# Performance work log

Measured on AMD Instinct MI355X. Metric: run time of the kernel, lower is better.

The kernel has to match this reference:

```python
import jax, jax.numpy as jnp
import numpy as np

H = 4096
T = 8192
EPS = 1e-06
BLK = 16  # NVFP4 block size (per-16-element fp8 block scales)

# representable magnitudes of FP4 e2m1 and midpoints for round-to-nearest
FP4_VALS = jnp.array([0.0, 0.5, 1.0, 1.5, 2.0, 3.0, 4.0, 6.0], dtype=jnp.float32)
FP4_MIDS = jnp.array([0.25, 0.75, 1.25, 1.75, 2.5, 3.5, 5.0], dtype=jnp.float32)
FP8_MAX = 448.0  # e4m3fn max


def fp4_round(x):
    """Round to nearest FP4 (e2m1) value, saturating at +/-6."""
    s = jnp.sign(x)
    a = jnp.clip(jnp.abs(x), 0.0, 6.0)
    idx = jnp.searchsorted(FP4_MIDS, a, side='right')
    return s * FP4_VALS[idx]


def fp4_quant(x, gs):
    """Emulates vllm scaled_fp4_quant: per-16-elem fp8(e4m3) block scales with a
    global fp32 scale gs. Returns (q_blocks [M, K/16, 16], scale [M, K/16, 1]).
    Dequant relation: x ~= q * scale / gs."""
    M, K = x.shape
    xb = x.reshape(M, K // BLK, BLK)
    amax = jnp.max(jnp.abs(xb), axis=-1, keepdims=True)
    sc = jnp.clip(amax / 6.0 * gs, 0.0, FP8_MAX)
    sc = sc.astype(jnp.float8_e4m3fn).astype(jnp.float32)  # fp8 rounding of block scale
    safe_sc = jnp.where(sc > 0, sc, 1.0)
    q = fp4_round(jnp.where(sc > 0, xb * gs / safe_sc, 0.0))
    return q, sc


def fp4_mm(aq, asc, bq, bsc, alpha):
    """Emulates cutlass_scaled_fp4_mm: out = (Aq*asc) @ (Bq*bsc)^T * alpha,
    where alpha = 1/(a_global_scale * b_global_scale)."""
    M = aq.shape[0]
    N = bq.shape[0]
    A = (aq * asc).reshape(M, -1)
    B = (bq * bsc).reshape(N, -1)
    return (A @ B.T) * alpha


def rmsnorm(x, w, eps=EPS):
    return x * jax.lax.rsqrt(jnp.mean(x * x, axis=-1, keepdims=True) + eps) * w


def setup_inputs() -> dict:
    key = jax.random.key(0)
    ks = jax.random.split(key, 5)
    hidden_states = jax.random.normal(ks[0], (T, H), dtype=jnp.float32)
    norm_w = jax.random.uniform(ks[1], (4, H), dtype=jnp.float32)
    w = jax.random.uniform(ks[2], (3, H, H), dtype=jnp.float32)
    agscale = jax.random.uniform(ks[3], (3,), dtype=jnp.float32)
    wgscale = jax.random.uniform(ks[4], (3,), dtype=jnp.float32)
    return dict(hidden_states=hidden_states, norm_w=norm_w, w=w,
                agscale=agscale, wgscale=wgscale)


def reference(hidden_states, norm_w, w, agscale, wgscale):
    # tensor_model_parallel_all_reduce is identity on a single device
    x = jax.nn.relu(hidden_states)
    resid = x
    y = rmsnorm(x, norm_w[0])
    for i in range(3):
        wq, wsc = fp4_quant(w[i], wgscale[i])      # weight quant (done at init in torch)
        yq, ysc = fp4_quant(y, agscale[i])          # activation static quant
        alpha = 1.0 / (wgscale[i] * agscale[i])
        z = fp4_mm(yq, ysc, wq, wsc, alpha)         # [T, H]
        x = z + resid                                # fused add RMSNorm
        resid = x
        y = rmsnorm(x, norm_w[i + 1])
    return y
```

## Files before the change

### kernel.cpp

```cpp
#include <hip/hip_runtime.h>

constexpr int HD = 4096;
constexpr int TD = 8192;

typedef __bf16 bf16;
typedef __bf16 bf16x4 __attribute__((ext_vector_type(4)));
typedef __bf16 bf16x8 __attribute__((ext_vector_type(8)));
typedef float  f32x4  __attribute__((ext_vector_type(4)));

__device__ __forceinline__ float e4m3_round(float v) {
    if (!(v > 0.0f)) return 0.0f;
    unsigned b = __float_as_uint(v);
    int exp = (int)((b >> 23) & 255) - 127;
    int shift = (exp < -6) ? -9 : (exp - 3);
    float sc  = __uint_as_float((unsigned)(127 + shift) << 23);
    float isc = __uint_as_float((unsigned)(127 - shift) << 23);
    return rintf(v * isc) * sc;
}

__device__ __forceinline__ float fp4_round(float x) {
    float s = (x < 0.0f) ? -1.0f : 1.0f;
    float a = fminf(fabsf(x), 6.0f);
    float v;
    if      (a < 0.25f) v = 0.0f;
    else if (a < 0.75f) v = 0.5f;
    else if (a < 1.25f) v = 1.0f;
    else if (a < 1.75f) v = 1.5f;
    else if (a < 2.5f)  v = 2.0f;
    else if (a < 3.5f)  v = 3.0f;
    else if (a < 5.0f)  v = 4.0f;
    else                v = 6.0f;
    return s * v;
}

__device__ __forceinline__ void load_lds16(const void* g, void* l) {
    typedef __attribute__((address_space(1))) const void gv_t;
    typedef __attribute__((address_space(3))) void lv_t;
    __builtin_amdgcn_global_load_lds((gv_t*)g, (lv_t*)l, 16, 0, 0);
}

__global__ __launch_bounds__(256) void quant_w_kernel(
        const float* __restrict__ w, const float* __restrict__ wg,
        bf16* __restrict__ bdeq) {
    const size_t t4 = (size_t)blockIdx.x * 256 + threadIdx.x;
    const int mat = (int)(t4 >> 22);
    const float gs = wg[mat];
    const float4 v = ((const float4*)w)[t4];
    float am = fmaxf(fmaxf(fabsf(v.x), fabsf(v.y)), fmaxf(fabsf(v.z), fabsf(v.w)));
    am = fmaxf(am, __shfl_xor(am, 1));
    am = fmaxf(am, __shfl_xor(am, 2));
    const float sc = e4m3_round(fminf((am / 6.0f) * gs, 448.0f));
    bf16x4 o;
    if (sc > 0.0f) {
        o[0] = (bf16)(fp4_round(v.x * gs / sc) * sc);
        o[1] = (bf16)(fp4_round(v.y * gs / sc) * sc);
        o[2] = (bf16)(fp4_round(v.z * gs / sc) * sc);
        o[3] = (bf16)(fp4_round(v.w * gs / sc) * sc);
    } else {
        o[0] = o[1] = o[2] = o[3] = (bf16)0.0f;
    }
    ((bf16x4*)bdeq)[t4] = o;
}

__global__ __launch_bounds__(256) void rms_quant_kernel(
        const float* __restrict__ in, float* __restrict__ resid_out,
        const float* __restrict__ nw, const float* __restrict__ gsp,
        bf16* __restrict__ qout, float* __restrict__ yout, const int mode) {
    const int row  = blockIdx.x;
    const int tid  = threadIdx.x;
    const int lane = tid & 63;
    const int wave = tid >> 6;
    const float* x = in + (size_t)row * HD;

    float4 v[4];
    float ss = 0.0f;
#pragma unroll
    for (int c = 0; c < 4; c++) {
        v[c] = ((const float4*)x)[c * 256 + tid];
        if (mode == 0) {
            v[c].x = fmaxf(v[c].x, 0.0f);
            v[c].y = fmaxf(v[c].y, 0.0f);
            v[c].z = fmaxf(v[c].z, 0.0f);
            v[c].w = fmaxf(v[c].w, 0.0f);
        }
        ss += v[c].x * v[c].x + v[c].y * v[c].y + v[c].z * v[c].z + v[c].w * v[c].w;
    }
    if (mode == 0) {
        float4* r = (float4*)(resid_out + (size_t)row * HD);
#pragma unroll
        for (int c = 0; c < 4; c++) r[c * 256 + tid] = v[c];
    }
#pragma unroll
    for (int m = 1; m < 64; m <<= 1) ss += __shfl_xor(ss, m);
    __shared__ float sred[4];
    if (lane == 0) sred[wave] = ss;
    __syncthreads();
    const float total = sred[0] + sred[1] + sred[2] + sred[3];
    const float rs = rsqrtf(total * (1.0f / HD) + 1e-6f);
    const float gs = (mode == 2) ? 0.0f : *gsp;

#pragma unroll
    for (int c = 0; c < 4; c++) {
        const float4 nv = ((const float4*)nw)[c * 256 + tid];
        float4 y;
        y.x = v[c].x * rs * nv.x;
        y.y = v[c].y * rs * nv.y;
        y.z = v[c].z * rs * nv.z;
        y.w = v[c].w * rs * nv.w;
        if (mode == 2) {
            ((float4*)(yout + (size_t)row * HD))[c * 256 + tid] = y;
        } else {
            float am = fmaxf(fmaxf(fabsf(y.x), fabsf(y.y)), fmaxf(fabsf(y.z), fabsf(y.w)));
            am = fmaxf(am, __shfl_xor(am, 1));
            am = fmaxf(am, __shfl_xor(am, 2));
            const float sc = e4m3_round(fminf((am / 6.0f) * gs, 448.0f));
            bf16x4 o;
            if (sc > 0.0f) {
                o[0] = (bf16)(fp4_round(y.x * gs / sc) * sc);
                o[1] = (bf16)(fp4_round(y.y * gs / sc) * sc);
                o[2] = (bf16)(fp4_round(y.z * gs / sc) * sc);
                o[3] = (bf16)(fp4_round(y.w * gs / sc) * sc);
            } else {
                o[0] = o[1] = o[2] = o[3] = (bf16)0.0f;
            }
            ((bf16x4*)(qout + (size_t)row * HD))[c * 256 + tid] = o;
        }
    }
}

__global__ __launch_bounds__(256) void gemm_bt_kernel(
        const bf16* __restrict__ A, const bf16* __restrict__ B,
        float* __restrict__ C,
        const float* __restrict__ agp, const float* __restrict__ wgp) {
    __shared__ __align__(16) bf16 sA[128 * 32];
    __shared__ __align__(16) bf16 sB[128 * 32];

    const int tid  = threadIdx.x;
    const int lane = tid & 63;
    const int wave = tid >> 6;
    const int tileM = blockIdx.x * 128;
    const int tileN = blockIdx.y * 128;
    const int waveM = (wave & 1) * 64;
    const int waveN = (wave >> 1) * 64;
    const int quad = lane >> 4;
    const int l16  = lane & 15;

    const float alpha = 1.0f / ((*wgp) * (*agp));

    f32x4 acc[4][4];
#pragma unroll
    for (int mi = 0; mi < 4; mi++)
#pragma unroll
        for (int ni = 0; ni < 4; ni++)
            acc[mi][ni] = (f32x4){0.0f, 0.0f, 0.0f, 0.0f};

    const int ch0 = tid,       row0 = ch0 >> 2, col0 = (ch0 & 3) * 8;
    const int ch1 = tid + 256, row1 = ch1 >> 2, col1 = (ch1 & 3) * 8;
    const bf16* gA0 = A + (size_t)(tileM + row0) * HD + col0;
    const bf16* gA1 = A + (size_t)(tileM + row1) * HD + col1;
    const bf16* gB0 = B + (size_t)(tileN + row0) * HD + col0;
    const bf16* gB1 = B + (size_t)(tileN + row1) * HD + col1;
    bf16* lA0 = &sA[(0 * 256 + wave * 64) * 8];
    bf16* lA1 = &sA[(1 * 256 + wave * 64) * 8];
    bf16* lB0 = &sB[(0 * 256 + wave * 64) * 8];
    bf16* lB1 = &sB[(1 * 256 + wave * 64) * 8];

    for (int k0 = 0; k0 < HD; k0 += 32) {
        load_lds16(gA0 + k0, lA0);
        load_lds16(gA1 + k0, lA1);
        load_lds16(gB0 + k0, lB0);
        load_lds16(gB1 + k0, lB1);
        __syncthreads();

        bf16x8 aF[4], bF[4];
#pragma unroll
        for (int mi = 0; mi < 4; mi++)
            aF[mi] = *(const bf16x8*)&sA[(waveM + mi * 16 + l16) * 32 + quad * 8];
#pragma unroll
        for (int ni = 0; ni < 4; ni++)
            bF[ni] = *(const bf16x8*)&sB[(waveN + ni * 16 + l16) * 32 + quad * 8];
#pragma unroll
        for (int mi = 0; mi < 4; mi++)
#pragma unroll
            for (int ni = 0; ni < 4; ni++)
                acc[mi][ni] = __builtin_amdgcn_mfma_f32_16x16x32_bf16(
                    aF[mi], bF[ni], acc[mi][ni], 0, 0, 0);
        __syncthreads();
    }

#pragma unroll
    for (int mi = 0; mi < 4; mi++) {
#pragma unroll
        for (int ni = 0; ni < 4; ni++) {
            const int col  = tileN + waveN + ni * 16 + l16;
            const int rowb = tileM + waveM + mi * 16 + quad * 4;
#pragma unroll
            for (int r = 0; r < 4; r++) {
                const size_t idx = (size_t)(rowb + r) * HD + col;
                C[idx] = acc[mi][ni][r] * alpha + C[idx];
            }
        }
    }
}

extern "C" void kernel_launch(void* const* d_in, const int* in_sizes, int n_in,
                              void* d_out, int out_size, void* d_ws, size_t ws_size,
                              hipStream_t stream) {
    const float* hidden = (const float*)d_in[0];
    const float* norm_w = (const float*)d_in[1];
    const float* w      = (const float*)d_in[2];
    const float* ag     = (const float*)d_in[3];
    const float* wg     = (const float*)d_in[4];
    float* out = (float*)d_out;

    char* ws = (char*)d_ws;
    bf16* Bdeq = (bf16*)ws;
    bf16* Adeq = (bf16*)(ws + (size_t)3 * HD * HD * 2);

    quant_w_kernel<<<(3 * HD * (HD / 4)) / 256, 256, 0, stream>>>(w, wg, Bdeq);

    rms_quant_kernel<<<TD, 256, 0, stream>>>(hidden, out, norm_w, ag, Adeq, nullptr, 0);

    const dim3 ggrid(TD / 128, HD / 128);
    for (int i = 0; i < 3; i++) {
        gemm_bt_kernel<<<ggrid, 256, 0, stream>>>(
            Adeq, Bdeq + (size_t)i * HD * HD, out, ag + i, wg + i);
        if (i < 2) {
            rms_quant_kernel<<<TD, 256, 0, stream>>>(
                out, nullptr, norm_w + (size_t)(i + 1) * HD, ag + (i + 1),
                Adeq, nullptr, 1);
        } else {
            rms_quant_kernel<<<TD, 256, 0, stream>>>(
                out, nullptr, norm_w + (size_t)3 * HD, nullptr,
                nullptr, out, 2);
        }
    }
    (void)in_sizes; (void)n_in; (void)out_size; (void)ws_size;
}
```

Baseline: 1.794 ms.

## Rewrite GEMM with 256x256 tiles, 4-stage LDS pipeline and swizzled layout

Replaces the 128x128 single-buffered bf16 GEMM with a 512-thread 256x256 tile kernel. It uses a 4-deep global-to-LDS prefetch ring with explicit vmcnt waits, XOR-swizzled LDS addressing to avoid bank conflicts, split A/B staging interleaved with MFMA phases under setprio, and a block-index swizzle for L2 locality. The aim is to hide load latency and raise data reuse per tile. The cost is much higher register and LDS pressure (128KB of LDS per block) and hand-tuned barrier and wait counts that are fragile.

```diff
diff --git a/kernel.cpp b/kernel.cpp
--- a/kernel.cpp
+++ b/kernel.cpp
@@ -128,74 +128,130 @@
     }
 }
 
-__global__ __launch_bounds__(256) void gemm_bt_kernel(
+__global__ __launch_bounds__(512, 2) void gemm_bt_kernel(
         const bf16* __restrict__ A, const bf16* __restrict__ B,
         float* __restrict__ C,
         const float* __restrict__ agp, const float* __restrict__ wgp) {
-    __shared__ __align__(16) bf16 sA[128 * 32];
-    __shared__ __align__(16) bf16 sB[128 * 32];
+    __shared__ __align__(16) bf16 sA[4 * 8192];
+    __shared__ __align__(16) bf16 sB[4 * 8192];
+
+    constexpr int NT = HD / 32;
 
     const int tid  = threadIdx.x;
+    const int wave = tid >> 6;
     const int lane = tid & 63;
-    const int wave = tid >> 6;
-    const int tileM = blockIdx.x * 128;
-    const int tileN = blockIdx.y * 128;
-    const int waveM = (wave & 1) * 64;
-    const int waveN = (wave >> 1) * 64;
+    const int l16  = lane & 15;
     const int quad = lane >> 4;
-    const int l16  = lane & 15;
+    const int wr   = wave >> 2;
+    const int wc   = wave & 3;
+
+    const int bid = blockIdx.x;
+    const int swz = (bid & 7) * 64 + (bid >> 3);
+    const int tileM = (swz & 31) * 256;
+    const int tileN = (swz >> 5) * 256;
 
     const float alpha = 1.0f / ((*wgp) * (*agp));
 
-    f32x4 acc[4][4];
-#pragma unroll
-    for (int mi = 0; mi < 4; mi++)
-#pragma unroll
-        for (int ni = 0; ni < 4; ni++)
+    f32x4 acc[8][4];
+#pragma unroll
+    for (int mi = 0; mi < 8; ++mi)
+#pragma unroll
+        for (int ni = 0; ni < 4; ++ni)
             acc[mi][ni] = (f32x4){0.0f, 0.0f, 0.0f, 0.0f};
 
-    const int ch0 = tid,       row0 = ch0 >> 2, col0 = (ch0 & 3) * 8;
-    const int ch1 = tid + 256, row1 = ch1 >> 2, col1 = (ch1 & 3) * 8;
-    const bf16* gA0 = A + (size_t)(tileM + row0) * HD + col0;
-    const bf16* gA1 = A + (size_t)(tileM + row1) * HD + col1;
-    const bf16* gB0 = B + (size_t)(tileN + row0) * HD + col0;
-    const bf16* gB1 = B + (size_t)(tileN + row1) * HD + col1;
-    bf16* lA0 = &sA[(0 * 256 + wave * 64) * 8];
-    bf16* lA1 = &sA[(1 * 256 + wave * 64) * 8];
-    bf16* lB0 = &sB[(0 * 256 + wave * 64) * 8];
-    bf16* lB1 = &sB[(1 * 256 + wave * 64) * 8];
-
-    for (int k0 = 0; k0 < HD; k0 += 32) {
-        load_lds16(gA0 + k0, lA0);
-        load_lds16(gA1 + k0, lA1);
-        load_lds16(gB0 + k0, lB0);
-        load_lds16(gB1 + k0, lB1);
-        __syncthreads();
-
-        bf16x8 aF[4], bF[4];
-#pragma unroll
-        for (int mi = 0; mi < 4; mi++)
-            aF[mi] = *(const bf16x8*)&sA[(waveM + mi * 16 + l16) * 32 + quad * 8];
-#pragma unroll
-        for (int ni = 0; ni < 4; ni++)
-            bF[ni] = *(const bf16x8*)&sB[(waveN + ni * 16 + l16) * 32 + quad * 8];
-#pragma unroll
-        for (int mi = 0; mi < 4; mi++)
-#pragma unroll
-            for (int ni = 0; ni < 4; ni++)
-                acc[mi][ni] = __builtin_amdgcn_mfma_f32_16x16x32_bf16(
-                    aF[mi], bF[ni], acc[mi][ni], 0, 0, 0);
-        __syncthreads();
-    }
-
-#pragma unroll
-    for (int mi = 0; mi < 4; mi++) {
-#pragma unroll
-        for (int ni = 0; ni < 4; ni++) {
-            const int col  = tileN + waveN + ni * 16 + l16;
-            const int rowb = tileM + waveM + mi * 16 + quad * 4;
-#pragma unroll
-            for (int r = 0; r < 4; r++) {
+    const int p0 = tid * 16;
+    const int p1 = 8192 + tid * 16;
+    const int q0 = p0 ^ (((p0 >> 7) & 3) << 4);
+    const int q1 = p1 ^ (((p1 >> 7) & 3) << 4);
+    const bf16* gA0 = A + (size_t)(tileM + (q0 >> 6)) * HD + ((q0 & 63) >> 1);
+    const bf16* gA1 = A + (size_t)(tileM + (q1 >> 6)) * HD + ((q1 & 63) >> 1);
+    const bf16* gB0 = B + (size_t)(tileN + (q0 >> 6)) * HD + ((q0 & 63) >> 1);
+    const bf16* gB1 = B + (size_t)(tileN + (q1 >> 6)) * HD + ((q1 & 63) >> 1);
+    char* const lA = (char*)sA + wave * 1024;
+    char* const lB = (char*)sB + wave * 1024;
+
+#define STAGE_A(b, k0) do {                                       \
+        load_lds16(gA0 + (k0), lA + (b) * 16384);                 \
+        load_lds16(gA1 + (k0), lA + (b) * 16384 + 8192); } while (0)
+#define STAGE_B(b, k0) do {                                       \
+        load_lds16(gB0 + (k0), lB + (b) * 16384);                 \
+        load_lds16(gB1 + (k0), lB + (b) * 16384 + 8192); } while (0)
+
+    const int fsw  = ((l16 >> 1) & 3) << 4;
+    const int offA = (((wr * 128 + l16) * 64 + quad * 16) ^ fsw);
+    const int offB = (((wc * 64  + l16) * 64 + quad * 16) ^ fsw);
+
+    bf16x8 aF[4], bF[4];
+
+#define READ_A(bufoff, mb) do { _Pragma("unroll")                              \
+        for (int mi = 0; mi < 4; ++mi)                                         \
+            aF[mi] = *(const bf16x8*)((const char*)sA + (bufoff) + offA +      \
+                                      ((mb) + mi) * 1024); } while (0)
+#define READ_B(bufoff) do { _Pragma("unroll")                                  \
+        for (int ni = 0; ni < 4; ++ni)                                         \
+            bF[ni] = *(const bf16x8*)((const char*)sB + (bufoff) + offB +      \
+                                      ni * 1024); } while (0)
+#define MFMA_Q(mb) do { _Pragma("unroll")                                      \
+        for (int mi = 0; mi < 4; ++mi) { _Pragma("unroll")                     \
+            for (int ni = 0; ni < 4; ++ni)                                     \
+                acc[(mb) + mi][ni] = __builtin_amdgcn_mfma_f32_16x16x32_bf16(  \
+                    aF[mi], bF[ni], acc[(mb) + mi][ni], 0, 0, 0); } } while (0)
+
+#define BAR()   __builtin_amdgcn_s_barrier()
+#define FENCE() asm volatile("" ::: "memory")
+
+    STAGE_A(0, 0);  STAGE_B(0, 0);
+    STAGE_A(1, 32); STAGE_B(1, 32);
+    STAGE_A(2, 64); STAGE_B(2, 64);
+    asm volatile("s_waitcnt vmcnt(8)" ::: "memory");
+    BAR(); FENCE();
+
+    for (int tt = 0; tt < NT - 3; ++tt) {
+        const int bufoff = (tt & 3) * 16384;
+        const int nb     = (tt + 3) & 3;
+        const int k0n    = (tt + 3) * 32;
+        STAGE_A(nb, k0n);
+        READ_A(bufoff, 0);
+        READ_B(bufoff);
+        BAR(); FENCE();
+        __builtin_amdgcn_s_setprio(1);
+        MFMA_Q(0);
+        __builtin_amdgcn_s_setprio(0);
+        BAR(); FENCE();
+        STAGE_B(nb, k0n);
+        READ_A(bufoff, 4);
+        BAR(); FENCE();
+        __builtin_amdgcn_s_setprio(1);
+        MFMA_Q(4);
+        __builtin_amdgcn_s_setprio(0);
+        asm volatile("s_waitcnt vmcnt(8)" ::: "memory");
+        BAR(); FENCE();
+    }
+
+#define TAIL_TILE(tt, WAITER) do {                                             \
+        const int bufoff = ((tt) & 3) * 16384;                                 \
+        READ_A(bufoff, 0); READ_B(bufoff);                                     \
+        BAR(); FENCE();                                                        \
+        __builtin_amdgcn_s_setprio(1); MFMA_Q(0); __builtin_amdgcn_s_setprio(0); \
+        BAR(); FENCE();                                                        \
+        READ_A(bufoff, 4);                                                     \
+        BAR(); FENCE();                                                        \
+        __builtin_amdgcn_s_setprio(1); MFMA_Q(4); __builtin_amdgcn_s_setprio(0); \
+        WAITER;                                                                \
+        BAR(); FENCE(); } while (0)
+
+    TAIL_TILE(NT - 3, asm volatile("s_waitcnt vmcnt(4)" ::: "memory"));
+    TAIL_TILE(NT - 2, asm volatile("s_waitcnt vmcnt(0)" ::: "memory"));
+    TAIL_TILE(NT - 1, );
+
+#pragma unroll
+    for (int mi = 0; mi < 8; ++mi) {
+#pragma unroll
+        for (int ni = 0; ni < 4; ++ni) {
+            const int col  = tileN + wc * 64 + ni * 16 + l16;
+            const int rowb = tileM + wr * 128 + mi * 16 + quad * 4;
+#pragma unroll
+            for (int r = 0; r < 4; ++r) {
                 const size_t idx = (size_t)(rowb + r) * HD + col;
                 C[idx] = acc[mi][ni][r] * alpha + C[idx];
             }
@@ -221,9 +277,8 @@
 
     rms_quant_kernel<<<TD, 256, 0, stream>>>(hidden, out, norm_w, ag, Adeq, nullptr, 0);
 
-    const dim3 ggrid(TD / 128, HD / 128);
     for (int i = 0; i < 3; i++) {
-        gemm_bt_kernel<<<ggrid, 256, 0, stream>>>(
+        gemm_bt_kernel<<<512, 512, 0, stream>>>(
             Adeq, Bdeq + (size_t)i * HD * HD, out, ag + i, wg + i);
         if (i < 2) {
             rms_quant_kernel<<<TD, 256, 0, stream>>>(
```

After: 1.674 ms. -6.7%, faster.
